# Performance work log

Measured on AMD Instinct MI355X. Metric: run time of the kernel, lower is better.

The kernel has to match this reference:

```python
import jax, jax.numpy as jnp
import numpy as np

B, T, DIM = 2, 2048, 2048
H, HKV = 16, 4
HD = DIM // H            # 128
KV_DIM = HKV * HD        # 512
ROPE_DIMS = 64           # partial rotation: only first 64 of 128 dims rotated
ROPE_BASE = 10000.0
RANK = 16


def setup_inputs() -> dict:
    key = jax.random.key(0)
    ks = jax.random.split(key, 15)
    n = lambda k, shape, scale: jax.random.normal(k, shape, jnp.float32) * scale
    d = {
        'x': n(ks[0], (B, T, DIM), 1.0),
        'Wq': n(ks[1], (DIM, DIM), DIM ** -0.5),
        'Wk': n(ks[2], (DIM, KV_DIM), DIM ** -0.5),
        'Wv': n(ks[3], (DIM, KV_DIM), DIM ** -0.5),
        'Wproj': n(ks[4], (DIM, DIM), DIM ** -0.5),
        'q_gain': jnp.ones((H,), jnp.float32),
        'q_A': n(ks[5], (DIM, RANK), DIM ** -0.5),
        'q_B': n(ks[6], (RANK, DIM), 0.02),
        'k_A': n(ks[7], (DIM, RANK), DIM ** -0.5),
        'k_B': n(ks[8], (RANK, KV_DIM), 0.02),
        'v_A': n(ks[9], (DIM, RANK), DIM ** -0.5),
        'v_B': n(ks[10], (RANK, KV_DIM), 0.02),
        'p_A': n(ks[11], (DIM, RANK), DIM ** -0.5),
        'p_B': n(ks[12], (RANK, DIM), 0.02),
    }
    return d


def _rope_cos_sin(seqlen, dtype):
    inv_freq = 1.0 / ROPE_BASE ** (jnp.arange(0, ROPE_DIMS, 2, dtype=jnp.float32) / ROPE_DIMS)
    freqs = jnp.arange(seqlen, dtype=jnp.float32)[:, None] * inv_freq[None, :]  # [T, 32]
    return jnp.cos(freqs).astype(dtype), jnp.sin(freqs).astype(dtype)


def _apply_rope(x, cos, sin):
    # x: [B, h, T, HD]; rotate only the first ROPE_DIMS dims
    x_rope, x_pass = x[..., :ROPE_DIMS], x[..., ROPE_DIMS:]
    half = ROPE_DIMS // 2
    x1, x2 = x_rope[..., :half], x_rope[..., half:]
    rot = jnp.concatenate([x1 * cos + x2 * sin, -x1 * sin + x2 * cos], axis=-1)
    return jnp.concatenate([rot, x_pass], axis=-1)


def _rms_norm(x):
    eps = jnp.finfo(x.dtype).eps
    return x * jax.lax.rsqrt(jnp.mean(x * x, axis=-1, keepdims=True) + eps)


def reference(x, Wq, Wk, Wv, Wproj, q_gain, q_A, q_B, k_A, k_B, v_A, v_B, p_A, p_B):
    bsz, seqlen, dim = x.shape
    group = H // HKV

    # QKV projections + LoRA adds
    q = x @ Wq + (x @ q_A) @ q_B                    # [B, T, DIM]
    k = x @ Wk + (x @ k_A) @ k_B                    # [B, T, KV_DIM]
    v = x @ Wv + (x @ v_A) @ v_B                    # [B, T, KV_DIM]

    q = q.reshape(bsz, seqlen, H, HD).transpose(0, 2, 1, 3)      # [B, H, T, D]
    k = k.reshape(bsz, seqlen, HKV, HD).transpose(0, 2, 1, 3)    # [B, Hkv, T, D]
    v = v.reshape(bsz, seqlen, HKV, HD).transpose(0, 2, 1, 3)

    q = _rms_norm(q)
    k = _rms_norm(k)

    cos, sin = _rope_cos_sin(seqlen, q.dtype)
    q = _apply_rope(q, cos, sin)
    k = _apply_rope(k, cos, sin)

    q = q * q_gain.astype(q.dtype)[None, :, None, None]

    # GQA attention: group query heads over shared kv heads
    qg = q.reshape(bsz, HKV, group, seqlen, HD)
    scale = HD ** -0.5
    scores = jnp.einsum('bkgtd,bksd->bkgts', qg, k) * scale      # [B, Hkv, g, T, T]
    causal = jnp.tril(jnp.ones((seqlen, seqlen), bool))
    scores = jnp.where(causal, scores, -jnp.inf)
    attn = jax.nn.softmax(scores, axis=-1)
    y = jnp.einsum('bkgts,bksd->bkgtd', attn, v)                 # [B, Hkv, g, T, D]

    # XSA: subtract self-value projection (GQA-aware)
    y_g = y.transpose(0, 3, 1, 2, 4)                              # [B, T, Hkv, g, D]
    v_bt = v.transpose(0, 2, 1, 3)                                # [B, T, Hkv, D]
    norm = jnp.sqrt(jnp.sum(v_bt * v_bt, axis=-1, keepdims=True))
    vn = (v_bt / jnp.maximum(norm, 1e-12))[:, :, :, None, :]      # [B, T, Hkv, 1, D]
    proj = jnp.sum(y_g * vn, axis=-1, keepdims=True) * vn
    y_out = (y_g - proj).reshape(bsz, seqlen, dim)

    out = y_out @ Wproj + (y_out @ p_A) @ p_B
    return out
```

## Files before the change

### kernel.cpp

```cpp
#include <hip/hip_runtime.h>

typedef unsigned short u16;
typedef __attribute__((ext_vector_type(4))) float f32x4;
typedef __attribute__((ext_vector_type(8))) short s16x8;
typedef __attribute__((ext_vector_type(4))) u16 u16x4;

#define AS1 __attribute__((address_space(1)))
#define AS3 __attribute__((address_space(3)))

__device__ inline u16 f2bf(float f) {
  union { float f; unsigned u; } v; v.f = f;
  unsigned r = v.u + 0x7FFFu + ((v.u >> 16) & 1u);
  return (u16)(r >> 16);
}
__device__ inline float bf2f(u16 h) {
  union { unsigned u; float f; } v; v.u = ((unsigned)h) << 16; return v.f;
}

__device__ inline float redsum16(float v) {
  v += __shfl_xor(v, 1); v += __shfl_xor(v, 2);
  v += __shfl_xor(v, 4); v += __shfl_xor(v, 8);
  return v;
}
__device__ inline float redsum64(float v) {
  v += __shfl_xor(v, 1); v += __shfl_xor(v, 2); v += __shfl_xor(v, 4);
  v += __shfl_xor(v, 8); v += __shfl_xor(v, 16); v += __shfl_xor(v, 32);
  return v;
}

__global__ void cast_x_kernel(const float* __restrict__ x, u16* __restrict__ xbf, int n4) {
  int i = blockIdx.x * blockDim.x + threadIdx.x;
  if (i < n4) {
    f32x4 v = ((const f32x4*)x)[i];
    u16x4 o; o.x = f2bf(v.x); o.y = f2bf(v.y); o.z = f2bf(v.z); o.w = f2bf(v.w);
    ((u16x4*)xbf)[i] = o;
  }
}

__global__ void rope_table_kernel(float* __restrict__ cosT, float* __restrict__ sinT) {
  int idx = blockIdx.x * 256 + threadIdx.x;
  int t = idx >> 5, i = idx & 31;
  float invf = (float)pow(10000.0, -(double)i / 32.0);
  float freq = (float)t * invf;
  cosT[idx] = (float)cos((double)freq);
  sinT[idx] = (float)sin((double)freq);
}

__global__ void fuse_w_kernel(const float* __restrict__ W, const float* __restrict__ A,
                              const float* __restrict__ Bl, u16* __restrict__ dstT, int N) {
  __shared__ float tile[32][33];
  int k0 = blockIdx.x * 32, n0 = blockIdx.y * 32;
  int tx = threadIdx.x, ty = threadIdx.y;
  #pragma unroll
  for (int i = 0; i < 4; i++) {
    int row = k0 + ty + i * 8;
    float s = W[(size_t)row * N + n0 + tx];
    #pragma unroll
    for (int r = 0; r < 16; r++) s += A[row * 16 + r] * Bl[r * N + n0 + tx];
    tile[ty + i * 8][tx] = s;
  }
  __syncthreads();
  #pragma unroll
  for (int i = 0; i < 4; i++) {
    int n = n0 + ty + i * 8;
    dstT[(size_t)n * 2048 + k0 + tx] = f2bf(tile[tx][ty + i * 8]);
  }
}

__global__ __launch_bounds__(256) void gemm_kernel(const u16* __restrict__ A,
    const u16* __restrict__ BT, float* __restrict__ C, int M, int N, int K) {
  __shared__ __attribute__((aligned(16))) u16 As[128 * 32];
  __shared__ __attribute__((aligned(16))) u16 Bs[128 * 32];
  const int tid = threadIdx.x;
  const int lane = tid & 63, wave = tid >> 6;
  const int wr = wave >> 1, wc = wave & 1;
  const int m0 = blockIdx.x * 128, n0 = blockIdx.y * 128;
  f32x4 acc[4][4] = {};
  const int lrow = tid >> 2, lseg = tid & 3;
  for (int k0 = 0; k0 < K; k0 += 32) {
    __syncthreads();
    #pragma unroll
    for (int r = 0; r < 2; r++) {
      const u16* gA = A + (size_t)(m0 + r * 64 + lrow) * K + k0 + lseg * 8;
      __builtin_amdgcn_global_load_lds((const AS1 void*)gA,
          (AS3 void*)(As + r * 2048 + wave * 512), 16, 0, 0);
      const u16* gB = BT + (size_t)(n0 + r * 64 + lrow) * K + k0 + lseg * 8;
      __builtin_amdgcn_global_load_lds((const AS1 void*)gB,
          (AS3 void*)(Bs + r * 2048 + wave * 512), 16, 0, 0);
    }
    __syncthreads();
    s16x8 af[4], bfr[4];
    #pragma unroll
    for (int m = 0; m < 4; m++)
      af[m] = *(const s16x8*)(As + (wr * 64 + m * 16 + (lane & 15)) * 32 + (lane >> 4) * 8);
    #pragma unroll
    for (int n = 0; n < 4; n++)
      bfr[n] = *(const s16x8*)(Bs + (wc * 64 + n * 16 + (lane & 15)) * 32 + (lane >> 4) * 8);
    #pragma unroll
    for (int m = 0; m < 4; m++)
      #pragma unroll
      for (int n = 0; n < 4; n++)
        acc[m][n] = __builtin_amdgcn_mfma_f32_16x16x32_bf16(af[m], bfr[n], acc[m][n], 0, 0, 0);
  }
  #pragma unroll
  for (int m = 0; m < 4; m++) {
    int row = m0 + wr * 64 + m * 16 + (lane >> 4) * 4;
    #pragma unroll
    for (int n = 0; n < 4; n++) {
      int col = n0 + wc * 64 + n * 16 + (lane & 15);
      float* cp = C + (size_t)row * N + col;
      #pragma unroll
      for (int j = 0; j < 4; j++) cp[(size_t)j * N] = acc[m][n][j];
    }
  }
}

__global__ __launch_bounds__(256) void qkpost_kernel(const float* __restrict__ QKV,
    const float* __restrict__ cosT, const float* __restrict__ sinT,
    const float* __restrict__ qgain, u16* __restrict__ Qbf, u16* __restrict__ Kbf) {
  int bt = blockIdx.x; int b = bt >> 11, t = bt & 2047;
  int lane = threadIdx.x & 63, wave = threadIdx.x >> 6;
  for (int u = wave; u < 20; u += 4) {
    const float* src = (u < 16) ? (QKV + (size_t)bt * 3072 + u * 128)
                                : (QKV + (size_t)bt * 3072 + 2048 + (u - 16) * 128);
    float x0 = src[lane], x1 = src[lane + 64];
    float ss = redsum64(x0 * x0 + x1 * x1);
    float r = 1.0f / sqrtf(ss * (1.0f / 128.0f) + 1.1920929e-7f);
    x0 *= r; x1 *= r;
    float partner = __shfl_xor(x0, 32);
    int i = lane & 31;
    float c = cosT[t * 32 + i], s = sinT[t * 32 + i];
    x0 = x0 * c + ((lane < 32) ? partner * s : -partner * s);
    if (u < 16) {
      float g = qgain[u] * 0.08838834764831845f;
      x0 *= g; x1 *= g;
      u16* dst = Qbf + ((size_t)(b * 16 + u) * 2048 + t) * 128;
      dst[lane] = f2bf(x0); dst[lane + 64] = f2bf(x1);
    } else {
      u16* dst = Kbf + ((size_t)(b * 4 + (u - 16)) * 2048 + t) * 128;
      dst[lane] = f2bf(x0); dst[lane + 64] = f2bf(x1);
    }
  }
}

__global__ void transv_kernel(const float* __restrict__ QKV, u16* __restrict__ Vt) {
  __shared__ float tile[32][33];
  int t0 = blockIdx.x * 32, d0 = blockIdx.y * 32, bh = blockIdx.z;
  int b = bh >> 2, kh = bh & 3;
  int tx = threadIdx.x, ty = threadIdx.y;
  #pragma unroll
  for (int i = 0; i < 4; i++) {
    int t = t0 + ty + i * 8;
    tile[ty + i * 8][tx] = QKV[((size_t)(b * 2048 + t)) * 3072 + 2560 + kh * 128 + d0 + tx];
  }
  __syncthreads();
  #pragma unroll
  for (int i = 0; i < 4; i++) {
    int d = d0 + ty + i * 8;
    Vt[((size_t)bh * 128 + d) * 2048 + t0 + tx] = f2bf(tile[tx][ty + i * 8]);
  }
}

__device__ __forceinline__ void load_tile(const u16* Kg, const u16* Vg, int kv0,
    int tid, f32x4* kreg, f32x4* vreg) {
  #pragma unroll
  for (int it = 0; it < 4; it++) {
    int u = it * 256 + tid;
    kreg[it] = *(const f32x4*)(Kg + (size_t)(kv0 + (u >> 4)) * 128 + (u & 15) * 8);
    vreg[it] = *(const f32x4*)(Vg + (size_t)(u >> 3) * 2048 + kv0 + (u & 7) * 8);
  }
}
__device__ __forceinline__ void write_tile(u16* Ks, u16* Vts, int tid,
    const f32x4* kreg, const f32x4* vreg) {
  #pragma unroll
  for (int it = 0; it < 4; it++) {
    int u = it * 256 + tid;
    int krow = u >> 4, kseg = u & 15;
    *(f32x4*)((char*)Ks + ((krow * 256 + kseg * 16) ^ ((krow & 7) << 4))) = kreg[it];
    int d = u >> 3, vseg = u & 7;
    *(f32x4*)((char*)Vts + ((d * 128 + vseg * 16) ^ ((d & 7) << 4))) = vreg[it];
  }
}

__device__ __forceinline__ void attn_step(const s16x8* qf, f32x4* yacc,
    float* l_part, const u16* Ks, const u16* Vts, u16* Pbuf,
    int kv0, int qbase, int lane, int wave, bool diag, float m_st) {
  f32x4 S[4];
  __builtin_amdgcn_s_setprio(1);
  #pragma unroll
  for (int nb = 0; nb < 4; nb++) {
    int kcol = nb * 16 + (lane & 15);
    f32x4 s = {};
    #pragma unroll
    for (int kb = 0; kb < 4; kb++) {
      int byt = (kcol * 256 + kb * 64 + (lane >> 4) * 16) ^ ((kcol & 7) << 4);
      s16x8 kf = *(const s16x8*)((const char*)Ks + byt);
      s = __builtin_amdgcn_mfma_f32_16x16x32_bf16(qf[kb], kf, s, 0, 0, 0);
    }
    S[nb] = s;
  }
  __builtin_amdgcn_s_setprio(0);
  if (diag) {
    #pragma unroll
    for (int nb = 0; nb < 4; nb++) {
      int kcol = kv0 + nb * 16 + (lane & 15);
      #pragma unroll
      for (int jj = 0; jj < 4; jj++) {
        int qr = qbase + wave * 16 + (lane >> 4) * 4 + jj;
        if (kcol > qr) S[nb][jj] = -1e30f;
      }
    }
  }
  #pragma unroll
  for (int nb = 0; nb < 4; nb++) {
    #pragma unroll
    for (int jj = 0; jj < 4; jj++) {
      float pv = __expf(S[nb][jj] - m_st);
      l_part[jj] += pv;
      int prow = (lane >> 4) * 4 + jj, pcol = nb * 16 + (lane & 15);
      int pbyte = (prow * 128 + pcol * 2) ^ ((prow & 7) << 4);
      *(u16*)((char*)Pbuf + pbyte) = f2bf(pv);
    }
  }
  s16x8 pa[2];
  #pragma unroll
  for (int k2 = 0; k2 < 2; k2++) {
    int prow = lane & 15;
    int pbyte = (prow * 128 + k2 * 64 + (lane >> 4) * 16) ^ ((prow & 7) << 4);
    pa[k2] = *(const s16x8*)((const char*)Pbuf + pbyte);
  }
  __builtin_amdgcn_s_setprio(1);
  #pragma unroll
  for (int nb = 0; nb < 8; nb++) {
    f32x4 y = yacc[nb];
    #pragma unroll
    for (int k2 = 0; k2 < 2; k2++) {
      int d = nb * 16 + (lane & 15);
      int vbyte = (d * 128 + k2 * 64 + (lane >> 4) * 16) ^ ((d & 7) << 4);
      s16x8 vf = *(const s16x8*)((const char*)Vts + vbyte);
      y = __builtin_amdgcn_mfma_f32_16x16x32_bf16(pa[k2], vf, y, 0, 0, 0);
    }
    yacc[nb] = y;
  }
  __builtin_amdgcn_s_setprio(0);
}

__global__ __launch_bounds__(256, 2) void attn_kernel(
    const u16* __restrict__ Qbf, const u16* __restrict__ Kbf,
    const u16* __restrict__ Vt, const float* __restrict__ qgain,
    u16* __restrict__ Ybf) {
  __shared__ __attribute__((aligned(16))) u16 Ks[2][64 * 128];
  __shared__ __attribute__((aligned(16))) u16 Vts[2][128 * 64];
  __shared__ __attribute__((aligned(16))) u16 Pl[4][2][1024];
  int p = blockIdx.x, h = blockIdx.y, b = blockIdx.z;
  int kh = h >> 2;
  int tid = threadIdx.x, lane = tid & 63, wave = tid >> 6;
  const int qiA = p, qiB = 31 - p;
  const int qbaseA = qiA * 64, qbaseB = qiB * 64;
  const u16* Qg = Qbf + ((size_t)(b * 16 + h) * 2048) * 128;
  const u16* Kg = Kbf + ((size_t)(b * 4 + kh) * 2048) * 128;
  const u16* Vg = Vt + ((size_t)(b * 4 + kh) * 128) * 2048;
  const float m_st = 11.427f * fabsf(qgain[h]);
  int qrA = qbaseA + wave * 16 + (lane & 15);
  int qrB = qbaseB + wave * 16 + (lane & 15);
  s16x8 qfA[4], qfB[4];
  #pragma unroll
  for (int kb = 0; kb < 4; kb++) {
    qfA[kb] = *(const s16x8*)(Qg + (size_t)qrA * 128 + kb * 32 + (lane >> 4) * 8);
    qfB[kb] = *(const s16x8*)(Qg + (size_t)qrB * 128 + kb * 32 + (lane >> 4) * 8);
  }
  f32x4 yA[8] = {}, yB[8] = {};
  float lA[4] = {}, lB[4] = {};
  f32x4 kreg[4], vreg[4];
  const int jmax = qiB;
  load_tile(Kg, Vg, 0, tid, kreg, vreg);
  write_tile(&Ks[0][0], &Vts[0][0], tid, kreg, vreg);
  load_tile(Kg, Vg, 64, tid, kreg, vreg);
  __syncthreads();
  for (int j = 0; j <= jmax; j++) {
    int cur = j & 1, kv0 = j * 64;
    if (j < jmax) {
      write_tile(&Ks[cur ^ 1][0], &Vts[cur ^ 1][0], tid, kreg, vreg);
      if (j + 2 <= jmax) load_tile(Kg, Vg, (j + 2) * 64, tid, kreg, vreg);
    }
    attn_step(qfB, yB, lB, &Ks[cur][0], &Vts[cur][0], &Pl[wave][1][0],
              kv0, qbaseB, lane, wave, j == qiB, m_st);
    if (j <= qiA)
      attn_step(qfA, yA, lA, &Ks[cur][0], &Vts[cur][0], &Pl[wave][0][0],
                kv0, qbaseA, lane, wave, j == qiA, m_st);
    __syncthreads();
  }
  #pragma unroll
  for (int jj = 0; jj < 4; jj++) {
    float linvB = 1.0f / redsum16(lB[jj]);
    int qr = qbaseB + wave * 16 + (lane >> 4) * 4 + jj;
    size_t ybase = ((size_t)(b * 16 + h) * 2048 + qr) * 128;
    #pragma unroll
    for (int nb = 0; nb < 8; nb++)
      Ybf[ybase + nb * 16 + (lane & 15)] = f2bf(yB[nb][jj] * linvB);
  }
  #pragma unroll
  for (int jj = 0; jj < 4; jj++) {
    float linvA = 1.0f / redsum16(lA[jj]);
    int qr = qbaseA + wave * 16 + (lane >> 4) * 4 + jj;
    size_t ybase = ((size_t)(b * 16 + h) * 2048 + qr) * 128;
    #pragma unroll
    for (int nb = 0; nb < 8; nb++)
      Ybf[ybase + nb * 16 + (lane & 15)] = f2bf(yA[nb][jj] * linvA);
  }
}

__global__ __launch_bounds__(256) void projrm_kernel(const float* __restrict__ QKV,
    const u16* __restrict__ Ybf, u16* __restrict__ Yout) {
  int bt = blockIdx.x;
  int b = bt >> 11, t = bt & 2047;
  int lane = threadIdx.x & 63, kh = threadIdx.x >> 6;
  const float* v = QKV + (size_t)bt * 3072 + 2560 + kh * 128;
  float v0 = v[lane], v1 = v[lane + 64];
  float sv = redsum64(v0 * v0 + v1 * v1);
  float denom = fmaxf(sqrtf(sv), 1e-12f);
  float inv2 = 1.0f / (denom * denom);
  #pragma unroll
  for (int g = 0; g < 4; g++) {
    int h = kh * 4 + g;
    const u16* y = Ybf + ((size_t)(b * 16 + h) * 2048 + t) * 128;
    float y0 = bf2f(y[lane]), y1 = bf2f(y[lane + 64]);
    float c = redsum64(y0 * v0 + y1 * v1) * inv2;
    u16* o = Yout + (size_t)bt * 2048 + h * 128;
    o[lane] = f2bf(y0 - c * v0);
    o[lane + 64] = f2bf(y1 - c * v1);
  }
}

extern "C" void kernel_launch(void* const* d_in, const int* in_sizes, int n_in,
                              void* d_out, int out_size, void* d_ws, size_t ws_size,
                              hipStream_t stream) {
  const float* x = (const float*)d_in[0];
  const float* Wq = (const float*)d_in[1];
  const float* Wk = (const float*)d_in[2];
  const float* Wv = (const float*)d_in[3];
  const float* Wp = (const float*)d_in[4];
  const float* qgain = (const float*)d_in[5];
  const float* qA = (const float*)d_in[6];
  const float* qB = (const float*)d_in[7];
  const float* kA = (const float*)d_in[8];
  const float* kB = (const float*)d_in[9];
  const float* vA = (const float*)d_in[10];
  const float* vB = (const float*)d_in[11];
  const float* pA = (const float*)d_in[12];
  const float* pB = (const float*)d_in[13];

  char* ws = (char*)d_ws;
  const size_t XBF  = 0;
  const size_t WQKV = 16777216;
  const size_t WPE  = 29360128;
  const size_t QKV  = 37748736;
  const size_t COS  = 88080384;
  const size_t SIN  = 88342528;
  const size_t QBF  = 88604672;
  const size_t KBF  = 105381888;
  const size_t VT   = 109576192;
  const size_t YBF  = 113770496;
  const size_t YOUT = 130547712;

  u16* xbf = (u16*)(ws + XBF);
  u16* wqkv = (u16*)(ws + WQKV);
  u16* wpe = (u16*)(ws + WPE);
  float* qkv = (float*)(ws + QKV);
  float* cosT = (float*)(ws + COS);
  float* sinT = (float*)(ws + SIN);
  u16* qbf = (u16*)(ws + QBF);
  u16* kbf = (u16*)(ws + KBF);
  u16* vt = (u16*)(ws + VT);
  u16* ybf = (u16*)(ws + YBF);
  u16* yout = (u16*)(ws + YOUT);

  cast_x_kernel<<<8192, 256, 0, stream>>>(x, xbf, 2097152);
  rope_table_kernel<<<256, 256, 0, stream>>>(cosT, sinT);
  fuse_w_kernel<<<dim3(64, 64), dim3(32, 8), 0, stream>>>(Wq, qA, qB, wqkv, 2048);
  fuse_w_kernel<<<dim3(64, 16), dim3(32, 8), 0, stream>>>(Wk, kA, kB, wqkv + (size_t)2048 * 2048, 512);
  fuse_w_kernel<<<dim3(64, 16), dim3(32, 8), 0, stream>>>(Wv, vA, vB, wqkv + (size_t)2560 * 2048, 512);
  fuse_w_kernel<<<dim3(64, 64), dim3(32, 8), 0, stream>>>(Wp, pA, pB, wpe, 2048);
  gemm_kernel<<<dim3(32, 24), 256, 0, stream>>>(xbf, wqkv, qkv, 4096, 3072, 2048);
  qkpost_kernel<<<4096, 256, 0, stream>>>(qkv, cosT, sinT, qgain, qbf, kbf);
  transv_kernel<<<dim3(64, 4, 8), dim3(32, 8), 0, stream>>>(qkv, vt);
  attn_kernel<<<dim3(16, 16, 2), 256, 0, stream>>>(qbf, kbf, vt, qgain, ybf);
  projrm_kernel<<<4096, 256, 0, stream>>>(qkv, ybf, yout);
  gemm_kernel<<<dim3(32, 16), 256, 0, stream>>>(yout, wpe, (float*)d_out, 4096, 2048, 2048);
}
```

Measured before the change: 413.2 us.

## Triple-buffer GEMM LDS loads with swizzle, XCD-aware block mapping, and MFMA priority

The bf16 MFMA GEMM now keeps three LDS stages and prefetches two k-tiles ahead. It waits with explicit vmcnt and s_barrier instead of a pair of __syncthreads per iteration, so global-to-LDS loads overlap the MFMA work. LDS columns are XOR-swizzled to cut bank conflicts on the fragment reads. Blocks are remapped on a 1D grid so that consecutive tiles land on the same XCD, and s_setprio raises wave priority around the MFMA loop. In exchange it uses three times the LDS and depends on hand-placed waitcnt counts being correct.

```diff
diff --git a/kernel.cpp b/kernel.cpp
--- a/kernel.cpp
+++ b/kernel.cpp
@@ -68,39 +68,74 @@
 }
 
 __global__ __launch_bounds__(256) void gemm_kernel(const u16* __restrict__ A,
-    const u16* __restrict__ BT, float* __restrict__ C, int M, int N, int K) {
-  __shared__ __attribute__((aligned(16))) u16 As[128 * 32];
-  __shared__ __attribute__((aligned(16))) u16 Bs[128 * 32];
+    const u16* __restrict__ BT, float* __restrict__ C, int M, int N, int K, int nn) {
+  __shared__ __attribute__((aligned(16))) u16 As[3][128 * 32];
+  __shared__ __attribute__((aligned(16))) u16 Bs[3][128 * 32];
   const int tid = threadIdx.x;
   const int lane = tid & 63, wave = tid >> 6;
   const int wr = wave >> 1, wc = wave & 1;
-  const int m0 = blockIdx.x * 128, n0 = blockIdx.y * 128;
+  const int cpx = gridDim.x >> 3;
+  const int wg = (blockIdx.x & 7) * cpx + (blockIdx.x >> 3);
+  const int m0 = (wg / nn) * 128, n0 = (wg % nn) * 128;
   f32x4 acc[4][4] = {};
-  const int lrow = tid >> 2, lseg = tid & 3;
-  for (int k0 = 0; k0 < K; k0 += 32) {
-    __syncthreads();
-    #pragma unroll
-    for (int r = 0; r < 2; r++) {
-      const u16* gA = A + (size_t)(m0 + r * 64 + lrow) * K + k0 + lseg * 8;
-      __builtin_amdgcn_global_load_lds((const AS1 void*)gA,
-          (AS3 void*)(As + r * 2048 + wave * 512), 16, 0, 0);
-      const u16* gB = BT + (size_t)(n0 + r * 64 + lrow) * K + k0 + lseg * 8;
-      __builtin_amdgcn_global_load_lds((const AS1 void*)gB,
-          (AS3 void*)(Bs + r * 2048 + wave * 512), 16, 0, 0);
-    }
-    __syncthreads();
+  const int NKT = K >> 5;
+  const int srow = tid >> 2, sslot = tid & 3;
+  const int scol0 = ((sslot ^ (srow & 3)) << 3);
+  const u16* gA0 = A + (size_t)(m0 + srow) * K + scol0;
+  const u16* gA1 = gA0 + (size_t)64 * K;
+  const u16* gB0 = BT + (size_t)(n0 + srow) * K + scol0;
+  const u16* gB1 = gB0 + (size_t)64 * K;
+  const int rslot = (((lane >> 4) ^ (lane & 3)) << 3);
+  const int arow = wr * 64 + (lane & 15);
+  const int brow = wc * 64 + (lane & 15);
+  #pragma unroll
+  for (int kt = 0; kt < 2; kt++) {
+    __builtin_amdgcn_global_load_lds((const AS1 void*)(gA0 + kt * 32),
+        (AS3 void*)(&As[kt][0] + wave * 512), 16, 0, 0);
+    __builtin_amdgcn_global_load_lds((const AS1 void*)(gA1 + kt * 32),
+        (AS3 void*)(&As[kt][2048] + wave * 512), 16, 0, 0);
+    __builtin_amdgcn_global_load_lds((const AS1 void*)(gB0 + kt * 32),
+        (AS3 void*)(&Bs[kt][0] + wave * 512), 16, 0, 0);
+    __builtin_amdgcn_global_load_lds((const AS1 void*)(gB1 + kt * 32),
+        (AS3 void*)(&Bs[kt][2048] + wave * 512), 16, 0, 0);
+  }
+  int buf = 0, sbuf = 2;
+  for (int kt = 0; kt < NKT; kt++) {
+    if (kt < NKT - 1) {
+      asm volatile("s_waitcnt vmcnt(4)" ::: "memory");
+    } else {
+      asm volatile("s_waitcnt vmcnt(0)" ::: "memory");
+    }
+    asm volatile("s_barrier" ::: "memory");
+    if (kt + 2 < NKT) {
+      const int ko = (kt + 2) * 32;
+      __builtin_amdgcn_global_load_lds((const AS1 void*)(gA0 + ko),
+          (AS3 void*)(&As[sbuf][0] + wave * 512), 16, 0, 0);
+      __builtin_amdgcn_global_load_lds((const AS1 void*)(gA1 + ko),
+          (AS3 void*)(&As[sbuf][2048] + wave * 512), 16, 0, 0);
+      __builtin_amdgcn_global_load_lds((const AS1 void*)(gB0 + ko),
+          (AS3 void*)(&Bs[sbuf][0] + wave * 512), 16, 0, 0);
+      __builtin_amdgcn_global_load_lds((const AS1 void*)(gB1 + ko),
+          (AS3 void*)(&Bs[sbuf][2048] + wave * 512), 16, 0, 0);
+    }
+    const u16* Ab = &As[buf][0];
+    const u16* Bb = &Bs[buf][0];
     s16x8 af[4], bfr[4];
     #pragma unroll
     for (int m = 0; m < 4; m++)
-      af[m] = *(const s16x8*)(As + (wr * 64 + m * 16 + (lane & 15)) * 32 + (lane >> 4) * 8);
+      af[m] = *(const s16x8*)(Ab + (arow + m * 16) * 32 + rslot);
     #pragma unroll
     for (int n = 0; n < 4; n++)
-      bfr[n] = *(const s16x8*)(Bs + (wc * 64 + n * 16 + (lane & 15)) * 32 + (lane >> 4) * 8);
+      bfr[n] = *(const s16x8*)(Bb + (brow + n * 16) * 32 + rslot);
+    __builtin_amdgcn_s_setprio(1);
     #pragma unroll
     for (int m = 0; m < 4; m++)
       #pragma unroll
       for (int n = 0; n < 4; n++)
         acc[m][n] = __builtin_amdgcn_mfma_f32_16x16x32_bf16(af[m], bfr[n], acc[m][n], 0, 0, 0);
+    __builtin_amdgcn_s_setprio(0);
+    sbuf = buf;
+    buf = (buf == 2) ? 0 : buf + 1;
   }
   #pragma unroll
   for (int m = 0; m < 4; m++) {
@@ -381,10 +416,10 @@
   fuse_w_kernel<<<dim3(64, 16), dim3(32, 8), 0, stream>>>(Wk, kA, kB, wqkv + (size_t)2048 * 2048, 512);
   fuse_w_kernel<<<dim3(64, 16), dim3(32, 8), 0, stream>>>(Wv, vA, vB, wqkv + (size_t)2560 * 2048, 512);
   fuse_w_kernel<<<dim3(64, 64), dim3(32, 8), 0, stream>>>(Wp, pA, pB, wpe, 2048);
-  gemm_kernel<<<dim3(32, 24), 256, 0, stream>>>(xbf, wqkv, qkv, 4096, 3072, 2048);
+  gemm_kernel<<<768, 256, 0, stream>>>(xbf, wqkv, qkv, 4096, 3072, 2048, 24);
   qkpost_kernel<<<4096, 256, 0, stream>>>(qkv, cosT, sinT, qgain, qbf, kbf);
   transv_kernel<<<dim3(64, 4, 8), dim3(32, 8), 0, stream>>>(qkv, vt);
   attn_kernel<<<dim3(16, 16, 2), 256, 0, stream>>>(qbf, kbf, vt, qgain, ybf);
   projrm_kernel<<<4096, 256, 0, stream>>>(qkv, ybf, yout);
-  gemm_kernel<<<dim3(32, 16), 256, 0, stream>>>(yout, wpe, (float*)d_out, 4096, 2048, 2048);
-}
+  gemm_kernel<<<512, 256, 0, stream>>>(yout, wpe, (float*)d_out, 4096, 2048, 2048, 16);
+}
```

Result: faster. 393.6 us (-4.7%).
